# Performance work log

Hardware: AMD Instinct MI355X
Metric: run time of the kernel (lower is better)

## Reference

```python
import jax, jax.numpy as jnp
import numpy as np

N_GRAPHS = 512  # number of graphs in the batch
S2S_STEPS = 3   # Set2Set processing_steps


def segment_softmax(e, seg, num_seg):
    m = jax.ops.segment_max(e, seg, num_segments=num_seg)
    ex = jnp.exp(e - m[seg])
    s = jax.ops.segment_sum(ex, seg, num_segments=num_seg)
    return ex / s[seg]


def setup_inputs() -> dict:
    key = jax.random.key(0)
    ks = jax.random.split(key, 24)
    N, E, Fin, Fe, D = 30000, 480000, 25, 14, 256
    s = 0.05
    inp = {
        "x": jax.random.normal(ks[0], (N, Fin), jnp.float32),
        "edge_attr": jax.random.normal(ks[1], (E, Fe), jnp.float32),
        # lin0
        "W0": jax.random.normal(ks[2], (Fin, D), jnp.float32) * s,
        "b0": jnp.zeros((D,), jnp.float32),
        # DMPNN edge-message MLP: [x_src || e_attr] -> D -> D
        "Wm1": jax.random.normal(ks[3], (D + Fe, D), jnp.float32) * s,
        "bm1": jnp.zeros((D,), jnp.float32),
        "Wm2": jax.random.normal(ks[4], (D, D), jnp.float32) * s,
        "bm2": jnp.zeros((D,), jnp.float32),
        # node (root) update
        "Wr": jax.random.normal(ks[5], (D, D), jnp.float32) * s,
        "br": jnp.zeros((D,), jnp.float32),
        # Set2Set LSTM: input 2D -> hidden D
        "Wih": jax.random.normal(ks[6], (2 * D, 4 * D), jnp.float32) * s,
        "Whh": jax.random.normal(ks[7], (D, 4 * D), jnp.float32) * s,
        "bl": jnp.zeros((4 * D,), jnp.float32),
        # readout MLP
        "W1": jax.random.normal(ks[8], (2 * D, D), jnp.float32) * s,
        "b1": jnp.zeros((D,), jnp.float32),
        "W2": jax.random.normal(ks[9], (D, 1), jnp.float32) * s,
        "b2": jnp.zeros((1,), jnp.float32),
        "edge_index": jax.random.randint(ks[10], (2, E), 0, N, jnp.int32),
        "batch": jnp.sort(jax.random.randint(ks[11], (N,), 0, N_GRAPHS, jnp.int32)),
    }
    return inp


def reference(x, edge_attr, W0, b0, Wm1, bm1, Wm2, bm2, Wr, br,
              Wih, Whh, bl, W1, b1, W2, b2, edge_index, batch):
    N = x.shape[0]
    # lin0 + relu
    h0 = jax.nn.relu(x @ W0 + b0)  # [N, D]
    # DMPNNLayer2: edge-conditioned message, sum-aggregate, root update (eval: no dropout)
    src, dst = edge_index[0], edge_index[1]
    m = jax.nn.relu(jnp.concatenate([h0[src], edge_attr], axis=-1) @ Wm1 + bm1)  # [E, D]
    m = m @ Wm2 + bm2
    agg = jax.ops.segment_sum(m, dst, num_segments=N)  # [N, D]
    out = jax.nn.relu(h0 @ Wr + br + agg)  # relu in top-level forward, massage_depth=1
    # Set2Set pooling (processing_steps=3)
    D = out.shape[1]
    B = N_GRAPHS
    q_star = jnp.zeros((B, 2 * D), out.dtype)
    h = jnp.zeros((B, D), out.dtype)
    c = jnp.zeros((B, D), out.dtype)
    for _ in range(S2S_STEPS):
        gates = q_star @ Wih + h @ Whh + bl  # [B, 4D]
        i, f, g, o = jnp.split(gates, 4, axis=-1)
        c = jax.nn.sigmoid(f) * c + jax.nn.sigmoid(i) * jnp.tanh(g)
        h = jax.nn.sigmoid(o) * jnp.tanh(c)
        e = jnp.sum(out * h[batch], axis=-1)              # [N]
        a = segment_softmax(e, batch, B)                  # [N]
        r = jax.ops.segment_sum(a[:, None] * out, batch, num_segments=B)  # [B, D]
        q_star = jnp.concatenate([h, r], axis=-1)
    # readout (eval: dropout identity)
    y = jax.nn.relu(q_star @ W1 + b1)
    y = y @ W2 + b2
    return y.reshape(-1)
```

## Files before the change

### kernel.cpp

```cpp
#include <hip/hip_runtime.h>

typedef unsigned short u16;
typedef unsigned char u8;
typedef unsigned int u32;
using s16x8 = __attribute__((ext_vector_type(8))) short;
using s16x4 = __attribute__((ext_vector_type(4))) short;
using f32x4 = __attribute__((ext_vector_type(4))) float;

#define DEV static __device__ __forceinline__

DEV float b2f(u16 u) { return __uint_as_float(((u32)u) << 16); }
DEV u16 f2bu(float f) {
    u32 u = __float_as_uint(f);
    u32 r = (u + 0x7FFFu + ((u >> 16) & 1u)) >> 16;
    return (u16)r;
}
DEV float sigm(float x) { return 1.0f / (1.0f + expf(-x)); }

DEV float ldv(const void* p, int i, int f32flag) {
    if (f32flag) return ((const float*)p)[i];
    return b2f(((const u16*)p)[i]);
}
DEV void stv(void* p, int i, float v, int f32flag) {
    if (f32flag) ((float*)p)[i] = v;
    else ((u16*)p)[i] = f2bu(v);
}

DEV int lower_bound(const int* b, int n, int v) {
    int lo = 0, hi = n;
    while (lo < hi) { int mid = (lo + hi) >> 1; if (b[mid] < v) lo = mid + 1; else hi = mid; }
    return lo;
}

__global__ void DMPNN_Change_678604832935_kernel(int* p) {
    if (p && threadIdx.x == 0 && blockIdx.x == 0) p[0] = 1;
}

__global__ void detect_kernel(const void* x, int* flag) {
    __shared__ int cnt[128];
    int tid = threadIdx.x;
    if (tid < 128) {
        u16 v = ((const u16*)x)[tid];
        int e = (v >> 7) & 0xFF;
        cnt[tid] = (e >= 100 && e <= 141) ? 1 : 0;
    }
    __syncthreads();
    if (tid == 0) {
        int s = 0;
        for (int i = 0; i < 128; ++i) s += cnt[i];
        flag[0] = (s < 110) ? 1 : 0;
    }
}

__global__ void fillv_kernel(void* out, const int* flag, float v) {
    int i = blockIdx.x * 256 + threadIdx.x;
    if (i < 512) stv(out, i, v, flag[0]);
}

__global__ void zero_kernel(float* p, int n) {
    int i = blockIdx.x * 256 + threadIdx.x;
    int stride = gridDim.x * 256;
    for (; i < n; i += stride) p[i] = 0.0f;
}

__global__ void hist_kernel(const int* __restrict__ eidx, u32* __restrict__ cnt) {
    int i = blockIdx.x * 256 + threadIdx.x;
    if (i < 480000) atomicAdd(&cnt[eidx[480000 + i]], 1u);
}

__global__ void scan1_kernel(const u32* __restrict__ cnt, u32* __restrict__ part) {
    __shared__ u32 s[256];
    int i = blockIdx.x * 256 + threadIdx.x;
    s[threadIdx.x] = (i < 30000) ? cnt[i] : 0u;
    __syncthreads();
    for (int st = 128; st > 0; st >>= 1) {
        if (threadIdx.x < st) s[threadIdx.x] += s[threadIdx.x + st];
        __syncthreads();
    }
    if (threadIdx.x == 0) part[blockIdx.x] = s[0];
}

__global__ void scan2_kernel(const u32* __restrict__ part, u32* __restrict__ pexcl, int nb) {
    if (threadIdx.x == 0 && blockIdx.x == 0) {
        u32 run = 0;
        for (int i = 0; i < nb; ++i) { pexcl[i] = run; run += part[i]; }
    }
}

__global__ void scan3_kernel(u32* __restrict__ cursor, const u32* __restrict__ pexcl) {
    __shared__ u32 s[256];
    int b = blockIdx.x, tid = threadIdx.x;
    int i = b * 256 + tid;
    u32 v = (i < 30000) ? cursor[i] : 0u;
    s[tid] = v;
    __syncthreads();
    for (int off = 1; off < 256; off <<= 1) {
        u32 t = (tid >= off) ? s[tid - off] : 0u;
        __syncthreads();
        s[tid] += t;
        __syncthreads();
    }
    u32 excl = s[tid] - v + pexcl[b];
    if (i < 30000) cursor[i] = excl;
}

__global__ void scatter_kernel(const int* __restrict__ eidx, u32* __restrict__ cursor,
                               u16* __restrict__ permLo, u8* __restrict__ permHi) {
    int i = blockIdx.x * 256 + threadIdx.x;
    if (i < 480000) {
        int d = eidx[480000 + i];
        u32 pos = atomicAdd(&cursor[d], 1u);
        permLo[pos] = (u16)(i & 0xFFFF);
        permHi[pos] = (u8)(i >> 16);
    }
}

__global__ void deg_kernel(const u32* __restrict__ cursor, float* __restrict__ degf) {
    int i = blockIdx.x * 256 + threadIdx.x;
    if (i < 30000) {
        u32 end = cursor[i];
        u32 beg = (i > 0) ? cursor[i - 1] : 0u;
        degf[i] = (float)(end - beg);
    }
}

__global__ void to_blocked(const void* src, int K, int ktiles, const int* flag,
                           u16* dst) {
    int idx = blockIdx.x * 256 + threadIdx.x;
    int total = ktiles * 4 * 256 * 8;
    if (idx >= total) return;
    int f32 = flag[0];
    int c = idx & 7;
    int n = (idx >> 3) & 255;
    int jk = idx >> 11;
    int j = jk & 3, kt = jk >> 2;
    int k = kt * 32 + j * 8 + c;
    u16 v = 0;
    if (k < K) v = f2bu(ldv(src, k * 256 + n, f32));
    dst[idx] = v;
}

__global__ void to_blocked2(const void* src1, int K1, const void* src2, int K2,
                            const int* flag, u16* dst) {
    int idx = blockIdx.x * 256 + threadIdx.x;
    int total = 24 * 4 * 1024 * 8;
    if (idx >= total) return;
    int f32 = flag[0];
    int c = idx & 7;
    int n = (idx >> 3) & 1023;
    int jk = idx >> 13;
    int j = jk & 3, kt = jk >> 2;
    int k = kt * 32 + j * 8 + c;
    u16 v = 0;
    if (k < K1) v = f2bu(ldv(src1, k * 1024 + n, f32));
    else if (k - K1 < K2) v = f2bu(ldv(src2, (k - K1) * 1024 + n, f32));
    dst[idx] = v;
}

__global__ __launch_bounds__(256) void lin0_kernel(const void* x, const void* W0,
                                                   const void* b0, const int* flag,
                                                   u16* h0b) {
    int f32 = flag[0];
    int n0 = blockIdx.x * 8, tid = threadIdx.x;
    __shared__ float xs[8][26];
    if (tid < 200) {
        int nn = tid / 25, k = tid % 25;
        xs[nn][k] = ldv(x, (n0 + nn) * 25 + k, f32);
    }
    __syncthreads();
    float wr[25];
    #pragma unroll
    for (int k = 0; k < 25; ++k) wr[k] = ldv(W0, k * 256 + tid, f32);
    float bias = ldv(b0, tid, f32);
    #pragma unroll
    for (int nn = 0; nn < 8; ++nn) {
        float a = bias;
        #pragma unroll
        for (int k = 0; k < 25; ++k) a += xs[nn][k] * wr[k];
        h0b[(n0 + nn) * 256 + tid] = f2bu(fmaxf(a, 0.0f));
    }
}

__global__ __launch_bounds__(256) void qgen_kernel(
    const u16* __restrict__ h0b, const u16* __restrict__ Wm1b,
    u16* __restrict__ Qb) {
    __shared__ __attribute__((aligned(16))) u16 As[64 * 264];
    const int tid = threadIdx.x;
    const int w = tid >> 6, lane = tid & 63, quad = lane >> 4, mrow = lane & 15;
    const int row0 = blockIdx.x * 64;
    const int colb = w * 64 + mrow;
    const int r = tid >> 2, sub = tid & 3;

    {
        int row = row0 + r;
        u16* arow = As + r * 264;
        #pragma unroll
        for (int j = 0; j < 8; ++j) {
            int c0 = sub * 64 + j * 8;
            s16x8 v = {0, 0, 0, 0, 0, 0, 0, 0};
            if (row < 30000) v = *(const s16x8*)(h0b + row * 256 + c0);
            *(s16x8*)(arow + c0) = v;
        }
    }
    __syncthreads();

    f32x4 acc[4][4];
    f32x4 fzero = {0.f, 0.f, 0.f, 0.f};
    #pragma unroll
    for (int mi = 0; mi < 4; ++mi)
        #pragma unroll
        for (int ni = 0; ni < 4; ++ni) acc[mi][ni] = fzero;

    for (int kt = 0; kt < 8; ++kt) {
        s16x8 af[4], bf[4];
        #pragma unroll
        for (int ni = 0; ni < 4; ++ni)
            bf[ni] = *(const s16x8*)(Wm1b + (((kt * 4 + quad) * 256) + colb + ni * 16) * 8);
        #pragma unroll
        for (int mi = 0; mi < 4; ++mi)
            af[mi] = *(const s16x8*)(As + (mi * 16 + mrow) * 264 + kt * 32 + quad * 8);
        #pragma unroll
        for (int mi = 0; mi < 4; ++mi)
            #pragma unroll
            for (int ni = 0; ni < 4; ++ni)
                acc[mi][ni] = __builtin_amdgcn_mfma_f32_16x16x32_bf16(af[mi], bf[ni], acc[mi][ni], 0, 0, 0);
    }

    #pragma unroll
    for (int mi = 0; mi < 4; ++mi)
        #pragma unroll
        for (int rg = 0; rg < 4; ++rg) {
            int row = row0 + mi * 16 + quad * 4 + rg;
            if (row >= 30000) continue;
            #pragma unroll
            for (int ni = 0; ni < 4; ++ni)
                Qb[row * 256 + colb + ni * 16] = f2bu(acc[mi][ni][rg]);
        }
}

#define MAXD 96
__global__ __launch_bounds__(256) void edge_mfma_node_kernel(
    const u16* __restrict__ Qb, const void* __restrict__ eattr,
    const int* __restrict__ eidx,
    const u16* __restrict__ permLo, const u8* __restrict__ permHi,
    const u32* __restrict__ cursor,
    const u16* __restrict__ Wm1b, const void* __restrict__ bm1,
    const int* __restrict__ flag, float* __restrict__ aggP) {
    const int f32 = flag[0];
    const int n = blockIdx.x, tid = threadIdx.x;
    const int w = tid >> 6, lane = tid & 63, quad = lane >> 4, mrow = lane & 15;
    const int beg = (n > 0) ? (int)cursor[n - 1] : 0;
    const int end = (int)cursor[n];
    __shared__ int eids[MAXD];
    __shared__ int sorted_s[MAXD];
    __shared__ int srcs16[16];
    __shared__ __attribute__((aligned(16))) u16 Ae[16 * 40];

    const int colb = w * 64 + mrow;
    s16x8 bf[4];
    float bm1c[4];
    #pragma unroll
    for (int ni = 0; ni < 4; ++ni) {
        bf[ni] = *(const s16x8*)(Wm1b + (((32 + quad) * 256) + colb + ni * 16) * 8);
        bm1c[ni] = ldv(bm1, colb + ni * 16, f32);
    }

    float psum[4] = {0.f, 0.f, 0.f, 0.f};
    const f32x4 fzero = {0.f, 0.f, 0.f, 0.f};

    for (int base = beg; base < end; base += MAXD) {
        int wcnt = end - base; if (wcnt > MAXD) wcnt = MAXD;
        if (tid < wcnt) {
            int si = base + tid;
            eids[tid] = (int)permLo[si] | ((int)permHi[si] << 16);
        }
        __syncthreads();
        if (tid < wcnt) {
            int key = eids[tid], r2 = 0;
            for (int j = 0; j < wcnt; ++j) r2 += (eids[j] < key);
            sorted_s[r2] = key;
        }
        __syncthreads();

        for (int cb = 0; cb < wcnt; cb += 16) {
            {
                int row = tid >> 4, c = tid & 15;
                int gi = cb + row;
                int e = (gi < wcnt) ? sorted_s[gi] : -1;
                u16 v = 0;
                if (e >= 0 && c < 14) v = f2bu(ldv(eattr, e * 14 + c, f32));
                Ae[row * 40 + c] = v;
                Ae[row * 40 + 16 + c] = 0;
                if (c == 0) srcs16[row] = (e >= 0) ? eidx[e] : 0;
            }
            __syncthreads();

            s16x8 af = *(const s16x8*)(Ae + mrow * 40 + quad * 8);
            f32x4 acc[4];
            #pragma unroll
            for (int ni = 0; ni < 4; ++ni)
                acc[ni] = __builtin_amdgcn_mfma_f32_16x16x32_bf16(af, bf[ni], fzero, 0, 0, 0);

            #pragma unroll
            for (int rg = 0; rg < 4; ++rg) {
                int row = quad * 4 + rg;
                if (cb + row < wcnt) {
                    const u16* qrow = Qb + srcs16[row] * 256;
                    #pragma unroll
                    for (int ni = 0; ni < 4; ++ni) {
                        float q = b2f(qrow[colb + ni * 16]);
                        psum[ni] += fmaxf(acc[ni][rg] + bm1c[ni] + q, 0.0f);
                    }
                }
            }
            __syncthreads();
        }
    }

    #pragma unroll
    for (int ni = 0; ni < 4; ++ni) {
        float v = psum[ni];
        v += __shfl_xor(v, 16, 64);
        v += __shfl_xor(v, 32, 64);
        psum[ni] = v;
    }
    if (quad == 0) {
        #pragma unroll
        for (int ni = 0; ni < 4; ++ni)
            aggP[n * 256 + colb + ni * 16] = psum[ni];
    }
}

__global__ __launch_bounds__(256) void edge_sorted_kernel(
    const u16* __restrict__ h0b, const void* __restrict__ eattr,
    const int* __restrict__ eidx,
    const u16* __restrict__ permLo, const u8* __restrict__ permHi,
    const u16* __restrict__ Wm1b,
    const void* __restrict__ bm1,
    const int* __restrict__ flag, float* __restrict__ aggP) {
    __shared__ __attribute__((aligned(16))) u16 As[64 * 296];
    __shared__ int dsh[64];
    const int f32 = flag[0];
    const int tid = threadIdx.x;
    const int w = tid >> 6, lane = tid & 63, quad = lane >> 4, mrow = lane & 15;
    const int eb0 = blockIdx.x * 64;
    const int colb = w * 64 + mrow;

    if (tid < 64) {
        int sj = eb0 + tid;
        int ee = (int)permLo[sj] | ((int)permHi[sj] << 16);
        dsh[tid] = eidx[480000 + ee];
    }
    {
        int r = tid >> 2, sub = tid & 3;
        int si = eb0 + r;
        int e = (int)permLo[si] | ((int)permHi[si] << 16);
        int src = eidx[e];
        const u16* hrow = h0b + src * 256;
        u16* arow = As + r * 296;
        #pragma unroll
        for (int j = 0; j < 8; ++j) {
            int c0 = sub * 64 + j * 8;
            *(s16x8*)(arow + c0) = *(const s16x8*)(hrow + c0);
        }
        if (sub == 0) {
            for (int c = 0; c < 14; ++c) arow[256 + c] = f2bu(ldv(eattr, e * 14 + c, f32));
            for (int c = 14; c < 40; ++c) arow[256 + c] = 0;
        }
    }
    __syncthreads();

    f32x4 acc[4][4];
    f32x4 fzero = {0.f, 0.f, 0.f, 0.f};
    #pragma unroll
    for (int mi = 0; mi < 4; ++mi)
        #pragma unroll
        for (int ni = 0; ni < 4; ++ni) acc[mi][ni] = fzero;

    for (int kt = 0; kt < 9; ++kt) {
        s16x8 af[4], bf[4];
        #pragma unroll
        for (int ni = 0; ni < 4; ++ni)
            bf[ni] = *(const s16x8*)(Wm1b + (((kt * 4 + quad) * 256) + colb + ni * 16) * 8);
        #pragma unroll
        for (int mi = 0; mi < 4; ++mi)
            af[mi] = *(const s16x8*)(As + (mi * 16 + mrow) * 296 + kt * 32 + quad * 8);
        #pragma unroll
        for (int mi = 0; mi < 4; ++mi)
            #pragma unroll
            for (int ni = 0; ni < 4; ++ni)
                acc[mi][ni] = __builtin_amdgcn_mfma_f32_16x16x32_bf16(af[mi], bf[ni], acc[mi][ni], 0, 0, 0);
    }

    float bm1c[4];
    #pragma unroll
    for (int ni = 0; ni < 4; ++ni) bm1c[ni] = ldv(bm1, colb + ni * 16, f32);
    __syncthreads();
    #pragma unroll
    for (int mi = 0; mi < 4; ++mi)
        #pragma unroll
        for (int ni = 0; ni < 4; ++ni)
            #pragma unroll
            for (int rg = 0; rg < 4; ++rg) {
                int row = mi * 16 + quad * 4 + rg;
                As[row * 296 + colb + ni * 16] = f2bu(fmaxf(acc[mi][ni][rg] + bm1c[ni], 0.0f));
            }
    __syncthreads();

    {
        int c = tid;
        float s = 0.0f;
        int cur = dsh[0];
        #pragma unroll 8
        for (int rr = 0; rr < 64; ++rr) {
            int d = dsh[rr];
            if (d != cur) { atomicAdd(&aggP[cur * 256 + c], s); s = 0.0f; cur = d; }
            s += b2f(As[rr * 296 + c]);
        }
        atomicAdd(&aggP[cur * 256 + c], s);
    }
}

__global__ __launch_bounds__(256) void node_dual_kernel(
    u16* __restrict__ h0b, const u16* __restrict__ Wrb, const u16* __restrict__ Wm2b,
    const void* __restrict__ br, const void* __restrict__ bm2,
    const float* __restrict__ aggP, const float* __restrict__ degf,
    const int* __restrict__ flag) {
    __shared__ __attribute__((aligned(16))) u16 As[64 * 264];
    const int f32 = flag[0];
    const int tid = threadIdx.x;
    const int w = tid >> 6, lane = tid & 63, quad = lane >> 4, mrow = lane & 15;
    const int row0 = blockIdx.x * 64;
    const int colb = w * 64 + mrow;
    const int r = tid >> 2, sub = tid & 3;

    {
        int row = row0 + r;
        u16* arow = As + r * 264;
        #pragma unroll
        for (int j = 0; j < 8; ++j) {
            int c0 = sub * 64 + j * 8;
            s16x8 v = {0, 0, 0, 0, 0, 0, 0, 0};
            if (row < 30000) v = *(const s16x8*)(h0b + row * 256 + c0);
            *(s16x8*)(arow + c0) = v;
        }
    }
    __syncthreads();

    f32x4 acc[4][4];
    f32x4 fzero = {0.f, 0.f, 0.f, 0.f};
    #pragma unroll
    for (int mi = 0; mi < 4; ++mi)
        #pragma unroll
        for (int ni = 0; ni < 4; ++ni) acc[mi][ni] = fzero;

    for (int kt = 0; kt < 8; ++kt) {
        s16x8 af[4], bf[4];
        #pragma unroll
        for (int ni = 0; ni < 4; ++ni)
            bf[ni] = *(const s16x8*)(Wrb + (((kt * 4 + quad) * 256) + colb + ni * 16) * 8);
        #pragma unroll
        for (int mi = 0; mi < 4; ++mi)
            af[mi] = *(const s16x8*)(As + (mi * 16 + mrow) * 264 + kt * 32 + quad * 8);
        #pragma unroll
        for (int mi = 0; mi < 4; ++mi)
            #pragma unroll
            for (int ni = 0; ni < 4; ++ni)
                acc[mi][ni] = __builtin_amdgcn_mfma_f32_16x16x32_bf16(af[mi], bf[ni], acc[mi][ni], 0, 0, 0);
    }
    __syncthreads();

    {
        int row = row0 + r;
        u16* arow = As + r * 264;
        #pragma unroll
        for (int j = 0; j < 8; ++j) {
            int c0 = sub * 64 + j * 8;
            s16x8 pk = {0, 0, 0, 0, 0, 0, 0, 0};
            if (row < 30000) {
                f32x4 a = *(const f32x4*)(aggP + row * 256 + c0);
                f32x4 b = *(const f32x4*)(aggP + row * 256 + c0 + 4);
                pk[0] = (short)f2bu(a[0]); pk[1] = (short)f2bu(a[1]);
                pk[2] = (short)f2bu(a[2]); pk[3] = (short)f2bu(a[3]);
                pk[4] = (short)f2bu(b[0]); pk[5] = (short)f2bu(b[1]);
                pk[6] = (short)f2bu(b[2]); pk[7] = (short)f2bu(b[3]);
            }
            *(s16x8*)(arow + c0) = pk;
        }
    }
    __syncthreads();

    for (int kt = 0; kt < 8; ++kt) {
        s16x8 af[4], bf[4];
        #pragma unroll
        for (int ni = 0; ni < 4; ++ni)
            bf[ni] = *(const s16x8*)(Wm2b + (((kt * 4 + quad) * 256) + colb + ni * 16) * 8);
        #pragma unroll
        for (int mi = 0; mi < 4; ++mi)
            af[mi] = *(const s16x8*)(As + (mi * 16 + mrow) * 264 + kt * 32 + quad * 8);
        #pragma unroll
        for (int mi = 0; mi < 4; ++mi)
            #pragma unroll
            for (int ni = 0; ni < 4; ++ni)
                acc[mi][ni] = __builtin_amdgcn_mfma_f32_16x16x32_bf16(af[mi], bf[ni], acc[mi][ni], 0, 0, 0);
    }

    #pragma unroll
    for (int mi = 0; mi < 4; ++mi)
        #pragma unroll
        for (int rg = 0; rg < 4; ++rg) {
            int row = row0 + mi * 16 + quad * 4 + rg;
            if (row >= 30000) continue;
            float dg = degf[row];
            #pragma unroll
            for (int ni = 0; ni < 4; ++ni) {
                int col = colb + ni * 16;
                float v = acc[mi][ni][rg] + ldv(br, col, f32) + dg * ldv(bm2, col, f32);
                h0b[row * 256 + col] = f2bu(fmaxf(v, 0.0f));
            }
        }
}

__global__ __launch_bounds__(256) void gates_mfma_kernel(
    const u16* __restrict__ Abuf, const u16* __restrict__ Wcatb,
    float* __restrict__ G) {
    const int tid = threadIdx.x;
    const int w = tid >> 6, lane = tid & 63, quad = lane >> 4, mrow = lane & 15;
    const int row0 = blockIdx.x * 64;
    const int col = blockIdx.y * 64 + w * 16 + mrow;

    f32x4 acc[4];
    f32x4 fzero = {0.f, 0.f, 0.f, 0.f};
    #pragma unroll
    for (int mi = 0; mi < 4; ++mi) acc[mi] = fzero;

    for (int kt = 0; kt < 24; ++kt) {
        s16x8 bfv = *(const s16x8*)(Wcatb + (((kt * 4 + quad) * 1024) + col) * 8);
        s16x8 af[4];
        #pragma unroll
        for (int mi = 0; mi < 4; ++mi)
            af[mi] = *(const s16x8*)(Abuf + (row0 + mi * 16 + mrow) * 768 + kt * 32 + quad * 8);
        #pragma unroll
        for (int mi = 0; mi < 4; ++mi)
            acc[mi] = __builtin_amdgcn_mfma_f32_16x16x32_bf16(af[mi], bfv, acc[mi], 0, 0, 0);
    }

    #pragma unroll
    for (int mi = 0; mi < 4; ++mi)
        #pragma unroll
        for (int rg = 0; rg < 4; ++rg)
            G[(row0 + mi * 16 + quad * 4 + rg) * 1024 + col] = acc[mi][rg];
}

__global__ __launch_bounds__(256) void lstm_kernel(const float* G, const void* bl,
                                                   const int* flag,
                                                   float* Cst, float* Hst,
                                                   u16* Abuf) {
    int f32 = flag[0];
    int b = blockIdx.x, d = threadIdx.x;
    float gi = G[b * 1024 + d]       + ldv(bl, d, f32);
    float gf = G[b * 1024 + 256 + d] + ldv(bl, 256 + d, f32);
    float gg = G[b * 1024 + 512 + d] + ldv(bl, 512 + d, f32);
    float go = G[b * 1024 + 768 + d] + ldv(bl, 768 + d, f32);
    float c = Cst[b * 256 + d];
    c = sigm(gf) * c + sigm(gi) * tanhf(gg);
    Cst[b * 256 + d] = c;
    float h = sigm(go) * tanhf(c);
    Hst[b * 256 + d] = h;
    u16 hb = f2bu(h);
    Abuf[b * 768 + d] = hb;
    Abuf[b * 768 + 512 + d] = hb;
}

#define GROWS 112
__global__ __launch_bounds__(256) void s2s_fused_kernel(
    const u16* __restrict__ outb, const float* __restrict__ Hst,
    const int* __restrict__ batch, float* __restrict__ Rst,
    u16* __restrict__ Abuf, float* __restrict__ ebuf) {
    __shared__ __attribute__((aligned(16))) u16 Ls[GROWS * 256];
    __shared__ __attribute__((aligned(16))) float hsh[256];
    __shared__ float esh[GROWS];
    __shared__ float red[256];
    const int b = blockIdx.x, tid = threadIdx.x;
    const int w = tid >> 6, lane = tid & 63;
    const int n0 = lower_bound(batch, 30000, b);
    const int n1 = lower_bound(batch, 30000, b + 1);
    const int cnt = n1 - n0;
    hsh[tid] = Hst[b * 256 + tid];
    __syncthreads();
    float r_out = 0.0f;
    if (cnt > 0 && cnt <= GROWS) {
        for (int idx = tid; idx < cnt * 32; idx += 256) {
            int i = idx >> 5, c8 = idx & 31;
            *(s16x8*)(Ls + i * 256 + c8 * 8) = *(const s16x8*)(outb + (n0 + i) * 256 + c8 * 8);
        }
        __syncthreads();
        for (int i = w; i < cnt; i += 4) {
            s16x4 ov = *(const s16x4*)(Ls + i * 256 + lane * 4);
            f32x4 hv = *(const f32x4*)(hsh + lane * 4);
            float p = b2f((u16)ov[0]) * hv[0] + b2f((u16)ov[1]) * hv[1]
                    + b2f((u16)ov[2]) * hv[2] + b2f((u16)ov[3]) * hv[3];
            #pragma unroll
            for (int off = 1; off < 64; off <<= 1) p += __shfl_xor(p, off, 64);
            if (lane == 0) esh[i] = p;
        }
        __syncthreads();
        float m = -1e30f;
        for (int i = tid; i < cnt; i += 256) m = fmaxf(m, esh[i]);
        red[tid] = m; __syncthreads();
        for (int s = 128; s > 0; s >>= 1) { if (tid < s) red[tid] = fmaxf(red[tid], red[tid + s]); __syncthreads(); }
        m = red[0]; __syncthreads();
        float sl = 0.0f;
        for (int i = tid; i < cnt; i += 256) { float pe = expf(esh[i] - m); esh[i] = pe; sl += pe; }
        red[tid] = sl; __syncthreads();
        for (int s = 128; s > 0; s >>= 1) { if (tid < s) red[tid] += red[tid + s]; __syncthreads(); }
        float ssum = red[0]; __syncthreads();
        float acc = 0.0f;
        for (int i = 0; i < cnt; ++i) acc += esh[i] * b2f(Ls[i * 256 + tid]);
        r_out = acc / ssum;
    } else if (cnt > GROWS) {
        for (int i = w; i < cnt; i += 4) {
            const u16* orow = outb + (n0 + i) * 256 + lane * 4;
            f32x4 hv = *(const f32x4*)(hsh + lane * 4);
            float p = b2f(orow[0]) * hv[0] + b2f(orow[1]) * hv[1]
                    + b2f(orow[2]) * hv[2] + b2f(orow[3]) * hv[3];
            #pragma unroll
            for (int off = 1; off < 64; off <<= 1) p += __shfl_xor(p, off, 64);
            if (lane == 0) ebuf[n0 + i] = p;
        }
        __syncthreads();
        float m = -1e30f;
        for (int n = n0 + tid; n < n1; n += 256) m = fmaxf(m, ebuf[n]);
        red[tid] = m; __syncthreads();
        for (int s = 128; s > 0; s >>= 1) { if (tid < s) red[tid] = fmaxf(red[tid], red[tid + s]); __syncthreads(); }
        m = red[0]; __syncthreads();
        float sl = 0.0f;
        for (int n = n0 + tid; n < n1; n += 256) sl += expf(ebuf[n] - m);
        red[tid] = sl; __syncthreads();
        for (int s = 128; s > 0; s >>= 1) { if (tid < s) red[tid] += red[tid + s]; __syncthreads(); }
        float ssum = red[0]; __syncthreads();
        float acc = 0.0f;
        for (int c0 = n0; c0 < n1; c0 += 256) {
            int nn = n1 - c0; if (nn > 256) nn = 256;
            __syncthreads();
            if (tid < nn) red[tid] = expf(ebuf[c0 + tid] - m);
            __syncthreads();
            for (int i = 0; i < nn; ++i) acc += red[i] * b2f(outb[(c0 + i) * 256 + tid]);
        }
        r_out = acc / ssum;
    }
    Rst[b * 256 + tid] = r_out;
    Abuf[b * 768 + 256 + tid] = f2bu(r_out);
}

__global__ __launch_bounds__(256) void readout_kernel(const float* Hst, const float* Rst,
                                                      const void* W1, const void* b1,
                                                      const void* W2, const void* b2,
                                                      const u16* nodeout, const float* aggP,
                                                      const int* flag, void* out) {
    int f32 = flag[0];
    int b = blockIdx.x, tid = threadIdx.x;
    __shared__ float qs[512];
    __shared__ float red[256];
    qs[tid] = Hst[b * 256 + tid];
    qs[256 + tid] = Rst[b * 256 + tid];
    __syncthreads();
    float a = ldv(b1, tid, f32);
    for (int k = 0; k < 512; ++k) a += qs[k] * ldv(W1, k * 256 + tid, f32);
    a = fmaxf(a, 0.0f) * ldv(W2, tid, f32);
    red[tid] = a; __syncthreads();
    for (int s = 128; s > 0; s >>= 1) { if (tid < s) red[tid] += red[tid + s]; __syncthreads(); }
    if (tid == 0) {
        float D = 0.0f;
        if (b == 0) {
            float s1 = 0.0f, s2 = 0.0f, s3 = 0.0f;
            for (int i = 0; i < 256; ++i) {
                s1 += fabsf(b2f(nodeout[i]));
                s2 += fabsf(aggP[i]);
                s3 += fabsf(Rst[i]);
            }
            if (s1 < 1e-3f) D += 100.0f;
            if (s2 < 1e-3f) D += 200.0f;
            if (s3 < 1e-6f) D += 400.0f;
        }
        stv(out, b, red[0] + ldv(b2, 0, f32) + D, f32);
    }
}

#define OFF_FLAG 0
#define OFF_HST  64
#define OFF_RST  524352
#define OFF_CST  1048640
#define OFF_PLO  64
#define OFF_PHI  960064
#define OFF_CUR  1440064
#define OFF_WREG 1572928
#define OFF_WM1B (OFF_WREG)
#define OFF_WM2B (OFF_WREG + 147456)
#define OFF_WRB  (OFF_WREG + 278528)
#define OFF_WCAT (OFF_WREG + 409600)
#define OFF_E    3670080
#define OFF_AGG  3790144
#define OFF_ABUF (OFF_AGG + 1048576)
#define OFF_G    (OFF_AGG + 4194304)
#define OFF_H0B  34510144
#define WS_NEEDED 49870144
#define OFF_Q    49870144
#define WS_FAST  (49870144 + 15360000)

extern "C" __attribute__((visibility("default")))
void kernel_launch(void* const* d_in, const int* in_sizes, int n_in,
                   void* d_out, int out_size, void* d_ws, size_t ws_size,
                   hipStream_t stream) {
    char* ws = (char*)d_ws;
    int*   flag   = (int*)(ws + OFF_FLAG);
    float* Hst    = (float*)(ws + OFF_HST);
    float* Rst    = (float*)(ws + OFF_RST);
    float* Cst    = (float*)(ws + OFF_CST);
    u16*   permLo = (u16*)(ws + OFF_PLO);
    u8*    permHi = (u8*)(ws + OFF_PHI);
    u32*   cursor = (u32*)(ws + OFF_CUR);
    u16*   Wm1b   = (u16*)(ws + OFF_WM1B);
    u16*   Wm2b   = (u16*)(ws + OFF_WM2B);
    u16*   Wrb    = (u16*)(ws + OFF_WRB);
    u16*   Wcatb  = (u16*)(ws + OFF_WCAT);
    float* ebuf   = (float*)(ws + OFF_E);
    u32*   part   = (u32*)(ws + OFF_E);
    u32*   pexcl  = (u32*)(ws + OFF_E + 512);
    float* degf   = (float*)(ws + OFF_E);
    float* aggP   = (float*)(ws + OFF_AGG);
    u16*   Abuf   = (u16*)(ws + OFF_ABUF);
    float* G      = (float*)(ws + OFF_G);
    u16*   h0b    = (u16*)(ws + OFF_H0B);
    u16*   Qb     = (u16*)(ws + OFF_Q);

    detect_kernel<<<1, 256, 0, stream>>>(d_in[0], flag);

    bool sizes_ok = (n_in == 19)
        && in_sizes[0] == 30000 * 25
        && in_sizes[1] == 480000 * 14
        && in_sizes[4] == 270 * 256
        && in_sizes[10] == 512 * 1024
        && in_sizes[17] == 2 * 480000
        && in_sizes[18] == 30000;
    if (!sizes_ok) { fillv_kernel<<<2, 256, 0, stream>>>(d_out, flag, 1600.0f); return; }
    if (ws_size < (size_t)WS_NEEDED) { fillv_kernel<<<2, 256, 0, stream>>>(d_out, flag, 800.0f); return; }
    const bool fast = (ws_size >= (size_t)WS_FAST);

    fillv_kernel<<<2, 256, 0, stream>>>(d_out, flag, 3.0f);
    DMPNN_Change_678604832935_kernel<<<1, 64, 0, stream>>>((int*)(ws + OFF_G));

    const void* x     = d_in[0];
    const void* eattr = d_in[1];
    const void* W0    = d_in[2];
    const void* b0    = d_in[3];
    const void* Wm1   = d_in[4];
    const void* bm1   = d_in[5];
    const void* Wm2   = d_in[6];
    const void* bm2   = d_in[7];
    const void* Wr    = d_in[8];
    const void* br    = d_in[9];
    const void* Wih   = d_in[10];
    const void* Whh   = d_in[11];
    const void* bl    = d_in[12];
    const void* W1    = d_in[13];
    const void* b1    = d_in[14];
    const void* W2    = d_in[15];
    const void* b2    = d_in[16];
    const int* eidx   = (const int*)d_in[17];
    const int* batch  = (const int*)d_in[18];

    to_blocked<<<288, 256, 0, stream>>>(Wm1, 270, 9, flag, Wm1b);
    to_blocked<<<256, 256, 0, stream>>>(Wm2, 256, 8, flag, Wm2b);
    to_blocked<<<256, 256, 0, stream>>>(Wr, 256, 8, flag, Wrb);
    to_blocked2<<<3072, 256, 0, stream>>>(Wih, 512, Whh, 256, flag, Wcatb);

    lin0_kernel<<<3750, 256, 0, stream>>>(x, W0, b0, flag, h0b);

    zero_kernel<<<30, 256, 0, stream>>>((float*)cursor, 30000);
    hist_kernel<<<1875, 256, 0, stream>>>(eidx, cursor);
    scan1_kernel<<<118, 256, 0, stream>>>(cursor, part);
    scan2_kernel<<<1, 64, 0, stream>>>(part, pexcl, 118);
    scan3_kernel<<<118, 256, 0, stream>>>(cursor, pexcl);
    scatter_kernel<<<1875, 256, 0, stream>>>(eidx, cursor, permLo, permHi);
    deg_kernel<<<118, 256, 0, stream>>>(cursor, degf);

    if (fast) {
        qgen_kernel<<<469, 256, 0, stream>>>(h0b, Wm1b, Qb);
        edge_mfma_node_kernel<<<30000, 256, 0, stream>>>(Qb, eattr, eidx, permLo, permHi,
                                                         cursor, Wm1b, bm1, flag, aggP);
    } else {
        zero_kernel<<<1024, 256, 0, stream>>>(aggP, 7680000);
        edge_sorted_kernel<<<7500, 256, 0, stream>>>(h0b, eattr, eidx, permLo, permHi,
                                                     Wm1b, bm1, flag, aggP);
    }
    node_dual_kernel<<<469, 256, 0, stream>>>(h0b, Wrb, Wm2b, br, bm2, aggP, degf, flag);

    zero_kernel<<<64, 256, 0, stream>>>(Cst, 131072);
    zero_kernel<<<64, 256, 0, stream>>>((float*)Abuf, 196608);

    for (int s = 0; s < 3; ++s) {
        gates_mfma_kernel<<<dim3(8, 16), 256, 0, stream>>>(Abuf, Wcatb, G);
        lstm_kernel<<<512, 256, 0, stream>>>(G, bl, flag, Cst, Hst, Abuf);
        s2s_fused_kernel<<<512, 256, 0, stream>>>(h0b, Hst, batch, Rst, Abuf, ebuf);
    }
    readout_kernel<<<512, 256, 0, stream>>>(Hst, Rst, W1, b1, W2, b2, h0b, aggP, flag, d_out);
}
```

Before: 506.3 us.

## Process dst-sorted edges in fixed 64-edge tiles with segmented atomic reduction

Replaces the one-block-per-node edge kernel (30000 blocks, per-node rank sort, 16-row MFMA chunks with padding waste) with fixed 64-edge tiles over the dst-sorted permutation. Each tile computes four MFMA row blocks, applies bias, Q and relu, then reduces each contiguous dst segment in registers and atomically adds it into aggP, which is now zeroed up front. This removes the load imbalance and idle lanes caused by variable degree, at the cost of float atomics (order-dependent summation) and a per-segment loop. The single-thread scan2 is also replaced by a wave-shuffle parallel scan.

```diff
diff --git a/kernel.cpp b/kernel.cpp
--- a/kernel.cpp
+++ b/kernel.cpp
@@ -81,10 +81,19 @@
 }
 
 __global__ void scan2_kernel(const u32* __restrict__ part, u32* __restrict__ pexcl, int nb) {
-    if (threadIdx.x == 0 && blockIdx.x == 0) {
-        u32 run = 0;
-        for (int i = 0; i < nb; ++i) { pexcl[i] = run; run += part[i]; }
-    }
+    int tid = threadIdx.x;
+    u32 v = (tid < nb) ? part[tid] : 0u;
+    u32 x = v;
+    #pragma unroll
+    for (int off = 1; off < 64; off <<= 1) {
+        u32 t = __shfl_up(x, off, 64);
+        if ((tid & 63) >= off) x += t;
+    }
+    __shared__ u32 wsum;
+    if (tid == 63) wsum = x;
+    __syncthreads();
+    u32 add = (tid >= 64) ? wsum : 0u;
+    if (tid < nb) pexcl[tid] = x + add - v;
 }
 
 __global__ void scan3_kernel(u32* __restrict__ cursor, const u32* __restrict__ pexcl) {
@@ -238,25 +247,50 @@
         }
 }
 
-#define MAXD 96
-__global__ __launch_bounds__(256) void edge_mfma_node_kernel(
+__global__ __launch_bounds__(256) void edge_qscan_kernel(
     const u16* __restrict__ Qb, const void* __restrict__ eattr,
     const int* __restrict__ eidx,
     const u16* __restrict__ permLo, const u8* __restrict__ permHi,
-    const u32* __restrict__ cursor,
     const u16* __restrict__ Wm1b, const void* __restrict__ bm1,
     const int* __restrict__ flag, float* __restrict__ aggP) {
+    __shared__ __attribute__((aligned(16))) u16 Ae[64 * 40];
+    __shared__ int eids[64];
+    __shared__ int srcs[64];
+    __shared__ int dsh[64];
+    __shared__ u8 segid_s[64];
+    __shared__ int segdst[64];
+    __shared__ int nseg_s;
     const int f32 = flag[0];
-    const int n = blockIdx.x, tid = threadIdx.x;
+    const int tid = threadIdx.x;
     const int w = tid >> 6, lane = tid & 63, quad = lane >> 4, mrow = lane & 15;
-    const int beg = (n > 0) ? (int)cursor[n - 1] : 0;
-    const int end = (int)cursor[n];
-    __shared__ int eids[MAXD];
-    __shared__ int sorted_s[MAXD];
-    __shared__ int srcs16[16];
-    __shared__ __attribute__((aligned(16))) u16 Ae[16 * 40];
-
+    const int eb0 = blockIdx.x * 64;
     const int colb = w * 64 + mrow;
+
+    if (tid < 64) {
+        int si = eb0 + tid;
+        int e = (int)permLo[si] | ((int)permHi[si] << 16);
+        eids[tid] = e;
+        srcs[tid] = eidx[e];
+        dsh[tid] = eidx[480000 + e];
+    }
+    __syncthreads();
+
+    if (tid < 64) {
+        int d = dsh[tid];
+        int fl = (tid == 0) || (d != dsh[tid - 1]);
+        unsigned long long mask = __ballot(fl);
+        int sid = (int)__popcll(mask & ((2ull << tid) - 1ull)) - 1;
+        segid_s[tid] = (u8)sid;
+        if (fl) segdst[sid] = d;
+        if (tid == 63) nseg_s = sid + 1;
+    }
+    for (int idx = tid; idx < 64 * 32; idx += 256) {
+        int row = idx >> 5, c = idx & 31;
+        u16 v = 0;
+        if (c < 14) v = f2bu(ldv(eattr, eids[row] * 14 + c, f32));
+        Ae[row * 40 + c] = v;
+    }
+
     s16x8 bf[4];
     float bm1c[4];
     #pragma unroll
@@ -264,70 +298,57 @@
         bf[ni] = *(const s16x8*)(Wm1b + (((32 + quad) * 256) + colb + ni * 16) * 8);
         bm1c[ni] = ldv(bm1, colb + ni * 16, f32);
     }
-
-    float psum[4] = {0.f, 0.f, 0.f, 0.f};
+    __syncthreads();
+
+    f32x4 acc[4][4];
     const f32x4 fzero = {0.f, 0.f, 0.f, 0.f};
-
-    for (int base = beg; base < end; base += MAXD) {
-        int wcnt = end - base; if (wcnt > MAXD) wcnt = MAXD;
-        if (tid < wcnt) {
-            int si = base + tid;
-            eids[tid] = (int)permLo[si] | ((int)permHi[si] << 16);
-        }
-        __syncthreads();
-        if (tid < wcnt) {
-            int key = eids[tid], r2 = 0;
-            for (int j = 0; j < wcnt; ++j) r2 += (eids[j] < key);
-            sorted_s[r2] = key;
-        }
-        __syncthreads();
-
-        for (int cb = 0; cb < wcnt; cb += 16) {
-            {
-                int row = tid >> 4, c = tid & 15;
-                int gi = cb + row;
-                int e = (gi < wcnt) ? sorted_s[gi] : -1;
-                u16 v = 0;
-                if (e >= 0 && c < 14) v = f2bu(ldv(eattr, e * 14 + c, f32));
-                Ae[row * 40 + c] = v;
-                Ae[row * 40 + 16 + c] = 0;
-                if (c == 0) srcs16[row] = (e >= 0) ? eidx[e] : 0;
+    #pragma unroll
+    for (int mi = 0; mi < 4; ++mi) {
+        s16x8 af = *(const s16x8*)(Ae + (mi * 16 + mrow) * 40 + quad * 8);
+        #pragma unroll
+        for (int ni = 0; ni < 4; ++ni)
+            acc[mi][ni] = __builtin_amdgcn_mfma_f32_16x16x32_bf16(af, bf[ni], fzero, 0, 0, 0);
+    }
+
+    int sid_r[4][4];
+    #pragma unroll
+    for (int mi = 0; mi < 4; ++mi)
+        #pragma unroll
+        for (int rg = 0; rg < 4; ++rg) {
+            int row = mi * 16 + quad * 4 + rg;
+            int src = srcs[row];
+            sid_r[mi][rg] = segid_s[row];
+            const u16* qrow = Qb + src * 256;
+            #pragma unroll
+            for (int ni = 0; ni < 4; ++ni)
+                acc[mi][ni][rg] = fmaxf(acc[mi][ni][rg] + bm1c[ni] + b2f(qrow[colb + ni * 16]), 0.0f);
+        }
+
+    int nseg = nseg_s;
+    for (int s = 0; s < nseg; ++s) {
+        float ps[4] = {0.f, 0.f, 0.f, 0.f};
+        #pragma unroll
+        for (int mi = 0; mi < 4; ++mi)
+            #pragma unroll
+            for (int rg = 0; rg < 4; ++rg) {
+                bool in = (sid_r[mi][rg] == s);
+                #pragma unroll
+                for (int ni = 0; ni < 4; ++ni)
+                    ps[ni] += in ? acc[mi][ni][rg] : 0.0f;
             }
-            __syncthreads();
-
-            s16x8 af = *(const s16x8*)(Ae + mrow * 40 + quad * 8);
-            f32x4 acc[4];
+        #pragma unroll
+        for (int ni = 0; ni < 4; ++ni) {
+            float v = ps[ni];
+            v += __shfl_xor(v, 16, 64);
+            v += __shfl_xor(v, 32, 64);
+            ps[ni] = v;
+        }
+        if (quad == 0) {
+            int d = segdst[s];
             #pragma unroll
             for (int ni = 0; ni < 4; ++ni)
-                acc[ni] = __builtin_amdgcn_mfma_f32_16x16x32_bf16(af, bf[ni], fzero, 0, 0, 0);
-
-            #pragma unroll
-            for (int rg = 0; rg < 4; ++rg) {
-                int row = quad * 4 + rg;
-                if (cb + row < wcnt) {
-                    const u16* qrow = Qb + srcs16[row] * 256;
-                    #pragma unroll
-                    for (int ni = 0; ni < 4; ++ni) {
-                        float q = b2f(qrow[colb + ni * 16]);
-                        psum[ni] += fmaxf(acc[ni][rg] + bm1c[ni] + q, 0.0f);
-                    }
-                }
-            }
-            __syncthreads();
-        }
-    }
-
-    #pragma unroll
-    for (int ni = 0; ni < 4; ++ni) {
-        float v = psum[ni];
-        v += __shfl_xor(v, 16, 64);
-        v += __shfl_xor(v, 32, 64);
-        psum[ni] = v;
-    }
-    if (quad == 0) {
-        #pragma unroll
-        for (int ni = 0; ni < 4; ++ni)
-            aggP[n * 256 + colb + ni * 16] = psum[ni];
+                atomicAdd(&aggP[d * 256 + colb + ni * 16], ps[ni]);
+        }
     }
 }
 
@@ -780,17 +801,17 @@
     zero_kernel<<<30, 256, 0, stream>>>((float*)cursor, 30000);
     hist_kernel<<<1875, 256, 0, stream>>>(eidx, cursor);
     scan1_kernel<<<118, 256, 0, stream>>>(cursor, part);
-    scan2_kernel<<<1, 64, 0, stream>>>(part, pexcl, 118);
+    scan2_kernel<<<1, 128, 0, stream>>>(part, pexcl, 118);
     scan3_kernel<<<118, 256, 0, stream>>>(cursor, pexcl);
     scatter_kernel<<<1875, 256, 0, stream>>>(eidx, cursor, permLo, permHi);
     deg_kernel<<<118, 256, 0, stream>>>(cursor, degf);
 
+    zero_kernel<<<1024, 256, 0, stream>>>(aggP, 7680000);
     if (fast) {
         qgen_kernel<<<469, 256, 0, stream>>>(h0b, Wm1b, Qb);
-        edge_mfma_node_kernel<<<30000, 256, 0, stream>>>(Qb, eattr, eidx, permLo, permHi,
-                                                         cursor, Wm1b, bm1, flag, aggP);
+        edge_qscan_kernel<<<7500, 256, 0, stream>>>(Qb, eattr, eidx, permLo, permHi,
+                                                    Wm1b, bm1, flag, aggP);
     } else {
-        zero_kernel<<<1024, 256, 0, stream>>>(aggP, 7680000);
         edge_sorted_kernel<<<7500, 256, 0, stream>>>(h0b, eattr, eidx, permLo, permHi,
                                                      Wm1b, bm1, flag, aggP);
     }
```

Result: slower. 539.5 us (+6.5%).
